# Performance work log

Hardware: AMD Instinct MI355X
Metric: run time of the kernel (lower is better)

## Reference

```python
import jax, jax.numpy as jnp
import numpy as np

M = 7          # init kwarg m
TAU = 3        # init kwarg tau
C_IN = 7       # init kwarg c_in
KSIZE = M + 1  # 8
NUM_KERNELS = 74
PAD = M * TAU  # 21, left-pad only
RAND_CH = 0    # original uses torch.randint at forward time; fixed for determinism


def setup_inputs() -> dict:
    key = jax.random.key(0)
    k1, k2 = jax.random.split(key)
    x = jax.random.normal(k1, (32, 8192, C_IN), dtype=jnp.float32)
    # learned parameter: self.kernels, shape [num_kernels, kernel_size]
    kernels = jax.random.normal(k2, (NUM_KERNELS, KSIZE), dtype=jnp.float32)
    return {"x": x, "kernels": kernels}


def reference(x, kernels):
    B, S, C = x.shape
    # pad left with zeros on time axis: [B, C, S+PAD]
    xp = jnp.pad(jnp.transpose(x, (0, 2, 1)), ((0, 0), (0, 0), (PAD, 0)))
    W = (S + PAD - KSIZE) // TAU + 1  # number of unfolded windows
    idx = jnp.arange(W)[:, None] * TAU + jnp.arange(KSIZE)[None, :]  # [W, K]
    windows = xp[:, :, idx]  # [B, C, W, K]
    # The 73-iteration depthwise conv1d loop (each output length 1) is exactly a
    # dot product of each window with each kernel. torch.cat over the loop is
    # kernel-major in the channel dim -> layout [B, W, n, C] -> [B, W, n*C].
    main = jnp.einsum('bcwk,nk->bwnc', windows, kernels[:NUM_KERNELS - 1])
    main = main.reshape(B, W, (NUM_KERNELS - 1) * C)
    # final feature: one selected channel convolved with the last kernel
    final = jnp.einsum('bwk,k->bw', windows[:, RAND_CH], kernels[-1])[..., None]
    combined = jnp.concatenate([main, final], axis=2)  # [B, W, 73*C+1]
    return jnp.transpose(combined, (0, 2, 1))[:, :, :S]
```

## Files before the change

### kernel.cpp

```cpp
#include <hip/hip_runtime.h>


typedef float f32x4 __attribute__((ext_vector_type(4)));

constexpr int Bn   = 32;
constexpr int Sn   = 8192;
constexpr int Cn   = 7;
constexpr int Kn   = 8;
constexpr int PADn = 21;
constexpr int Wn   = 2736;
constexpr int OCH  = 512;
constexpr int NCH  = 684;
constexpr int CHT  = 64;
constexpr int NWQ  = 11;
constexpr int SAMP = 773;
constexpr int CSTR = 776;

__global__ __launch_bounds__(256)
void conv_v5(const float* __restrict__ x, const float* __restrict__ kern,
             float* __restrict__ out) {
    __shared__ float lx[Cn * CSTR];

    const int tid = threadIdx.x;
    const int wq  = blockIdx.x;
    const int gp  = blockIdx.y;
    const int b   = blockIdx.z;

    const int sbase = wq * 768 - PADn;
    const int g0    = sbase * Cn;
    const float* xb = x + (size_t)b * Sn * Cn;
    for (int i = tid; i < SAMP * Cn; i += 256) {
        int gg = g0 + i;
        float v = (gg >= 0 && gg < Sn * Cn) ? xb[gg] : 0.0f;
        int s = i / 7;
        int c = i - 7 * s;
        lx[c * CSTR + s] = v;
    }
    __syncthreads();

    const int lane  = tid & 63;
    const int r     = __builtin_amdgcn_readfirstlane(tid >> 6);
    const int chunk = wq * CHT + lane;
    if (chunk >= NCH) return;

    const int n0 = gp ? 36 : 0;
    const int n1 = gp ? 73 : 36;

    float* ob = out + (size_t)b * OCH * Wn + 4 * chunk;
    const int sloc = 12 * lane;

    for (int c = 0; c < Cn; ++c) {
        const float* lr = lx + c * CSTR + sloc;
        float xw[17];
        *reinterpret_cast<f32x4*>(xw + 0)  = *reinterpret_cast<const f32x4*>(lr + 0);
        *reinterpret_cast<f32x4*>(xw + 4)  = *reinterpret_cast<const f32x4*>(lr + 4);
        *reinterpret_cast<f32x4*>(xw + 8)  = *reinterpret_cast<const f32x4*>(lr + 8);
        *reinterpret_cast<f32x4*>(xw + 12) = *reinterpret_cast<const f32x4*>(lr + 12);
        xw[16] = lr[16];

        for (int n = n0 + r; n < n1; n += 4) {
            const float* kr = kern + n * Kn;
            float a0 = 0.f, a1 = 0.f, a2 = 0.f, a3 = 0.f;
#pragma unroll
            for (int k = 0; k < 8; ++k) {
                float kv = kr[k];
                a0 = fmaf(xw[0 + k], kv, a0);
                a1 = fmaf(xw[3 + k], kv, a1);
                a2 = fmaf(xw[6 + k], kv, a2);
                a3 = fmaf(xw[9 + k], kv, a3);
            }
            f32x4 o = {a0, a1, a2, a3};
            *reinterpret_cast<f32x4*>(ob + (size_t)(n * 7 + c) * Wn) = o;
        }
        if (c == 0 && gp == 1 && r == 3) {
            const float* kr = kern + 73 * Kn;
            float a0 = 0.f, a1 = 0.f, a2 = 0.f, a3 = 0.f;
#pragma unroll
            for (int k = 0; k < 8; ++k) {
                float kv = kr[k];
                a0 = fmaf(xw[0 + k], kv, a0);
                a1 = fmaf(xw[3 + k], kv, a1);
                a2 = fmaf(xw[6 + k], kv, a2);
                a3 = fmaf(xw[9 + k], kv, a3);
            }
            f32x4 o = {a0, a1, a2, a3};
            *reinterpret_cast<f32x4*>(ob + (size_t)511 * Wn) = o;
        }
    }
}

extern "C" void kernel_launch(void* const* d_in, const int* in_sizes, int n_in,
                              void* d_out, int out_size, void* d_ws, size_t ws_size,
                              hipStream_t stream) {
    const float* x    = (const float*)d_in[0];
    const float* kern = (const float*)d_in[1];
    float* out        = (float*)d_out;

    conv_v5<<<dim3(NWQ, 2, Bn), 256, 0, stream>>>(x, kern, out);
}
```

Baseline: 39.88 us.

## Enlarge per-block time tile so each lane computes three chunks

Each block now covers a quarter of the windows (171 chunks) instead of 64, so each lane loads up to three input windows and reuses each kernel row's weights across three output chunks. The grid shrinks from 11x2x32 to 4x32x2 blocks, which cuts redundant halo loads and kernel reloads. In exchange, shared memory per block and register use per thread grow, and fewer blocks (256) may leave CUs underfilled on a large GPU. The third chunk is predicated for lanes past the tile edge.

```diff
diff --git a/kernel.cpp b/kernel.cpp
--- a/kernel.cpp
+++ b/kernel.cpp
@@ -10,24 +10,43 @@
 constexpr int PADn = 21;
 constexpr int Wn   = 2736;
 constexpr int OCH  = 512;
-constexpr int NCH  = 684;
-constexpr int CHT  = 64;
-constexpr int NWQ  = 11;
-constexpr int SAMP = 773;
-constexpr int CSTR = 776;
+constexpr int TW   = 684;
+constexpr int CHT  = 171;
+constexpr int SAMP = 2057;
+constexpr int CSTR = 2060;
+
+#define LOAD17(dst, src)                                                     \
+    *reinterpret_cast<f32x4*>((dst) + 0)  = *reinterpret_cast<const f32x4*>((src) + 0);  \
+    *reinterpret_cast<f32x4*>((dst) + 4)  = *reinterpret_cast<const f32x4*>((src) + 4);  \
+    *reinterpret_cast<f32x4*>((dst) + 8)  = *reinterpret_cast<const f32x4*>((src) + 8);  \
+    *reinterpret_cast<f32x4*>((dst) + 12) = *reinterpret_cast<const f32x4*>((src) + 12); \
+    (dst)[16] = (src)[16];
+
+#define PASS(dstp, xw, kv)                                                   \
+    {                                                                        \
+        float a0 = 0.f, a1 = 0.f, a2 = 0.f, a3 = 0.f;                        \
+        _Pragma("unroll")                                                    \
+        for (int k = 0; k < 8; ++k) {                                        \
+            a0 = fmaf((xw)[0 + k], (kv)[k], a0);                             \
+            a1 = fmaf((xw)[3 + k], (kv)[k], a1);                             \
+            a2 = fmaf((xw)[6 + k], (kv)[k], a2);                             \
+            a3 = fmaf((xw)[9 + k], (kv)[k], a3);                             \
+        }                                                                    \
+        f32x4 o = {a0, a1, a2, a3};                                          \
+        *reinterpret_cast<f32x4*>(dstp) = o;                                 \
+    }
 
 __global__ __launch_bounds__(256)
-void conv_v5(const float* __restrict__ x, const float* __restrict__ kern,
+void conv_v7(const float* __restrict__ x, const float* __restrict__ kern,
              float* __restrict__ out) {
     __shared__ float lx[Cn * CSTR];
 
     const int tid = threadIdx.x;
     const int wq  = blockIdx.x;
-    const int gp  = blockIdx.y;
-    const int b   = blockIdx.z;
+    const int b   = blockIdx.y;
+    const int gp  = blockIdx.z;
 
-    const int sbase = wq * 768 - PADn;
-    const int g0    = sbase * Cn;
+    const int g0 = (wq * (TW * 3) - PADn) * Cn;
     const float* xb = x + (size_t)b * Sn * Cn;
     for (int i = tid; i < SAMP * Cn; i += 256) {
         int gg = g0 + i;
@@ -38,53 +57,41 @@
     }
     __syncthreads();
 
-    const int lane  = tid & 63;
-    const int r     = __builtin_amdgcn_readfirstlane(tid >> 6);
-    const int chunk = wq * CHT + lane;
-    if (chunk >= NCH) return;
+    const int lane = tid & 63;
+    const int r    = __builtin_amdgcn_readfirstlane(tid >> 6);
+    const int n0   = gp ? 36 : 0;
+    const int n1   = gp ? 73 : 36;
+    const int ch0  = lane, ch1 = lane + 64, ch2 = lane + 128;
+    const bool p2  = (ch2 < CHT);
 
-    const int n0 = gp ? 36 : 0;
-    const int n1 = gp ? 73 : 36;
-
-    float* ob = out + (size_t)b * OCH * Wn + 4 * chunk;
-    const int sloc = 12 * lane;
+    float* ob = out + (size_t)b * OCH * Wn + 4 * (wq * CHT);
 
     for (int c = 0; c < Cn; ++c) {
-        const float* lr = lx + c * CSTR + sloc;
-        float xw[17];
-        *reinterpret_cast<f32x4*>(xw + 0)  = *reinterpret_cast<const f32x4*>(lr + 0);
-        *reinterpret_cast<f32x4*>(xw + 4)  = *reinterpret_cast<const f32x4*>(lr + 4);
-        *reinterpret_cast<f32x4*>(xw + 8)  = *reinterpret_cast<const f32x4*>(lr + 8);
-        *reinterpret_cast<f32x4*>(xw + 12) = *reinterpret_cast<const f32x4*>(lr + 12);
-        xw[16] = lr[16];
+        const float* lc = lx + c * CSTR;
+        float xw0[17], xw1[17], xw2[17];
+        LOAD17(xw0, lc + 12 * ch0)
+        LOAD17(xw1, lc + 12 * ch1)
+        if (p2) { LOAD17(xw2, lc + 12 * ch2) }
 
         for (int n = n0 + r; n < n1; n += 4) {
             const float* kr = kern + n * Kn;
-            float a0 = 0.f, a1 = 0.f, a2 = 0.f, a3 = 0.f;
+            float kv[8];
 #pragma unroll
-            for (int k = 0; k < 8; ++k) {
-                float kv = kr[k];
-                a0 = fmaf(xw[0 + k], kv, a0);
-                a1 = fmaf(xw[3 + k], kv, a1);
-                a2 = fmaf(xw[6 + k], kv, a2);
-                a3 = fmaf(xw[9 + k], kv, a3);
-            }
-            f32x4 o = {a0, a1, a2, a3};
-            *reinterpret_cast<f32x4*>(ob + (size_t)(n * 7 + c) * Wn) = o;
+            for (int k = 0; k < 8; ++k) kv[k] = kr[k];
+            float* orow = ob + (size_t)(n * 7 + c) * Wn;
+            PASS(orow + 4 * ch0, xw0, kv)
+            PASS(orow + 4 * ch1, xw1, kv)
+            if (p2) PASS(orow + 4 * ch2, xw2, kv)
         }
         if (c == 0 && gp == 1 && r == 3) {
             const float* kr = kern + 73 * Kn;
-            float a0 = 0.f, a1 = 0.f, a2 = 0.f, a3 = 0.f;
+            float kv[8];
 #pragma unroll
-            for (int k = 0; k < 8; ++k) {
-                float kv = kr[k];
-                a0 = fmaf(xw[0 + k], kv, a0);
-                a1 = fmaf(xw[3 + k], kv, a1);
-                a2 = fmaf(xw[6 + k], kv, a2);
-                a3 = fmaf(xw[9 + k], kv, a3);
-            }
-            f32x4 o = {a0, a1, a2, a3};
-            *reinterpret_cast<f32x4*>(ob + (size_t)511 * Wn) = o;
+            for (int k = 0; k < 8; ++k) kv[k] = kr[k];
+            float* orow = ob + (size_t)511 * Wn;
+            PASS(orow + 4 * ch0, xw0, kv)
+            PASS(orow + 4 * ch1, xw1, kv)
+            if (p2) PASS(orow + 4 * ch2, xw2, kv)
         }
     }
 }
@@ -96,5 +103,5 @@
     const float* kern = (const float*)d_in[1];
     float* out        = (float*)d_out;
 
-    conv_v5<<<dim3(NWQ, 2, Bn), 256, 0, stream>>>(x, kern, out);
+    conv_v7<<<dim3(4, Bn, 2), 256, 0, stream>>>(x, kern, out);
 }
```

Result: slower. 50.20 us (+25.9%).
